# Kernel optimization log

Hardware: AMD Instinct MI355X
Metric: run time of the kernel (lower is better)

## Reference

```python
import jax, jax.numpy as jnp
import numpy as np

B, N, D, H = 8, 512, 512, 8
DK = D // H          # 64
DIM_G = 64           # trigonometric geometry embedding dim
WAVE_LEN = 1000.0


def box_relational_embedding(f_g):
    # f_g: [B, N, 4] -> [B, N, N, 64]
    x_min, y_min, x_max, y_max = [f_g[..., i] for i in range(4)]  # [B,N]
    cx = (x_min + x_max) * 0.5
    cy = (y_min + y_max) * 0.5
    w = x_max - x_min + 1.0
    h = y_max - y_min + 1.0
    # pairwise deltas; divide by w_i / h_i of the row box (broadcast over j)
    dx = jnp.log(jnp.clip(jnp.abs((cx[:, :, None] - cx[:, None, :]) / w[:, :, None]), 0.001))
    dy = jnp.log(jnp.clip(jnp.abs((cy[:, :, None] - cy[:, None, :]) / h[:, :, None]), 0.001))
    dw = jnp.log(w[:, :, None] / w[:, None, :])
    dh = jnp.log(h[:, :, None] / h[:, None, :])
    pos = jnp.stack([dx, dy, dw, dh], axis=-1)  # [B,N,N,4]
    feat_range = jnp.arange(DIM_G // 8, dtype=jnp.float32) / (DIM_G / 8.0)  # [8]
    dim_mat = 1.0 / (WAVE_LEN ** feat_range)  # [8]
    mul = (100.0 * pos)[..., None] * dim_mat  # [B,N,N,4,8]
    mul = mul.reshape(pos.shape[0], pos.shape[1], pos.shape[2], -1)  # [B,N,N,32]
    return jnp.concatenate([jnp.sin(mul), jnp.cos(mul)], axis=-1)  # [B,N,N,64]


def setup_inputs() -> dict:
    key = jax.random.key(0)
    ks = jax.random.split(key, 12)
    s = 1.0 / np.sqrt(D)
    return {
        "input_query": jax.random.normal(ks[0], (B, N, D), jnp.float32),
        "input_key": jax.random.normal(ks[1], (B, N, D), jnp.float32),
        "input_value": jax.random.normal(ks[2], (B, N, D), jnp.float32),
        "input_box": jax.random.uniform(ks[3], (B, N, 4), jnp.float32),
        "mask": jax.random.randint(ks[4], (B, N), 0, 2, jnp.int32),
        "not_objects": jax.random.randint(ks[5], (B, N), 0, 2).astype(jnp.bool_),
        "Wq": jax.random.normal(ks[6], (D, D), jnp.float32) * s,
        "bq": jnp.zeros((D,), jnp.float32),
        "Wk": jax.random.normal(ks[7], (D, D), jnp.float32) * s,
        "bk": jnp.zeros((D,), jnp.float32),
        "Wv": jax.random.normal(ks[8], (D, D), jnp.float32) * s,
        "bv": jnp.zeros((D,), jnp.float32),
        "Wo": jax.random.normal(ks[9], (D, D), jnp.float32) * s,
        "bo": jnp.zeros((D,), jnp.float32),
        "WG": jax.random.normal(ks[10], (H, DIM_G), jnp.float32) * 0.1,
        "bG": jnp.zeros((H,), jnp.float32),
    }


def reference(input_query, input_key, input_value, input_box, mask, not_objects,
              Wq, bq, Wk, bk, Wv, bv, Wo, bo, WG, bG):
    emb = box_relational_embedding(input_box)  # [B,N,N,64]

    def proj(x, W, b):
        return (x @ W + b).reshape(B, N, H, DK).transpose(0, 2, 1, 3)  # [B,H,N,DK]

    q = proj(input_query, Wq, bq)
    k = proj(input_key, Wk, bk)
    v = proj(input_value, Wv, bv)

    scores = jnp.einsum('bhnd,bhmd->bhnm', q, k) / np.sqrt(DK).astype(np.float32)
    scores = jnp.where(mask[:, None, None, :] == 0, -1e9, scores)

    # per-head geometry weights: [B,H,N,N]
    wg = jax.nn.relu(jnp.einsum('bnmg,hg->bhnm', emb, WG) + bG[None, :, None, None])

    # object mask: zero the geometry log-bias where either i or j is not an object
    pair_not_obj = not_objects[:, None, :, None] | not_objects[:, None, None, :]  # [B,1,N,N]
    mask_obj = 1.0 - pair_not_obj.astype(jnp.float32)

    logits = jnp.log(jnp.clip(wg, 1e-6)) * mask_obj + scores
    attn = jax.nn.softmax(logits, axis=-1)  # dropout is identity in eval mode

    out = jnp.einsum('bhnm,bhmd->bhnd', attn, v)
    out = out.transpose(0, 2, 1, 3).reshape(B, N, D)
    return out @ Wo + bo
```

## Files before the change

### kernel.cpp

```cpp
#include <hip/hip_runtime.h>
#include <hip/hip_fp16.h>

#define B_ 8
#define N_ 512
#define D_ 512
#define H_ 8
#define DK_ 64

typedef unsigned int uint;
typedef unsigned short ushort;
typedef __attribute__((ext_vector_type(8))) short short8;
typedef __attribute__((ext_vector_type(8))) _Float16 half8;
typedef __attribute__((ext_vector_type(4))) _Float16 half4;
typedef __attribute__((ext_vector_type(4))) float floatx4;

__device__ __forceinline__ float bf2f(ushort s) { return __uint_as_float(((uint)s) << 16); }
__device__ __forceinline__ ushort f2bf(float f) {
    uint x = __float_as_uint(f);
    return (ushort)((x + 0x7fffu + ((x >> 16) & 1u)) >> 16);
}
__device__ __forceinline__ float blo(uint u) { return __uint_as_float(u << 16); }
__device__ __forceinline__ float bhi(uint u) { return __uint_as_float(u & 0xffff0000u); }
__device__ __forceinline__ float ldf(const void* p, size_t i, int isbf) {
    return isbf ? bf2f(((const ushort*)p)[i]) : ((const float*)p)[i];
}
__device__ __forceinline__ short ldb(const void* p, size_t i, int isbf) {
    return isbf ? (short)(((const ushort*)p)[i]) : (short)f2bf(((const float*)p)[i]);
}
__device__ __forceinline__ float4 ldbox(const void* p, size_t row, int isbf) {
    if (isbf) {
        const uint2 u = ((const uint2*)p)[row];
        return make_float4(blo(u.x), bhi(u.x), blo(u.y), bhi(u.y));
    }
    return ((const float4*)p)[row];
}
__device__ __forceinline__ float flog(float x) {
    return __builtin_amdgcn_logf(x) * 0.69314718056f;
}
__device__ __forceinline__ float fexp(float x) {
    return __builtin_amdgcn_exp2f(x * 1.44269504089f);
}
__device__ __forceinline__ void fsincos_rev(float rev, float* s, float* c) {
    const float fr = rev - floorf(rev);
    *s = __builtin_amdgcn_sinf(fr);
    *c = __builtin_amdgcn_cosf(fr);
}
__device__ __forceinline__ uint pkbf(uint a, uint b) {
    return __builtin_amdgcn_perm(b + 0x8000u, a + 0x8000u, 0x07060302u);
}
__device__ __forceinline__ int sniff_dtype(const uint* q, int* scratch) {
    const int t = threadIdx.x;
    int cnt = 0;
    for (int i = t; i < 4096; i += 256) {
        const uint e = (q[i] >> 7) & 0xffu;
        cnt += (e >= 0x70u && e <= 0x84u) ? 1 : 0;
    }
    scratch[t] = cnt;
    __syncthreads();
    for (int d = 128; d > 0; d >>= 1) {
        if (t < d) scratch[t] += scratch[t + d];
        __syncthreads();
    }
    const int r = (scratch[0] > 3276) ? 1 : 0;
    __syncthreads();
    return r;
}

__global__ __launch_bounds__(256) void probe_dtype(const uint* __restrict__ q,
                                                   int* __restrict__ flag) {
    __shared__ int s[256];
    const int r = sniff_dtype(q, s);
    if (threadIdx.x == 0) *flag = r;
}

__global__ __launch_bounds__(256) void transw(const void* __restrict__ w0,
                                              const void* __restrict__ w1,
                                              const void* __restrict__ w2,
                                              const void* __restrict__ w3,
                                              const void* __restrict__ b0,
                                              const void* __restrict__ b1,
                                              const void* __restrict__ b2,
                                              const void* __restrict__ b3,
                                              const uint* __restrict__ xq,
                                              ushort* __restrict__ wt,
                                              float* __restrict__ biasf,
                                              int* __restrict__ flag) {
    __shared__ int cnt_s[256];
    const int isbf = sniff_dtype(xq, cnt_s);
    const int z = blockIdx.z;
    const void* W = (z == 0) ? w0 : (z == 1) ? w1 : (z == 2) ? w2 : w3;
    const int n0 = blockIdx.x * 32, k0 = blockIdx.y * 32;
    __shared__ float tile[32][33];
    const int tx = threadIdx.x & 31, ty = threadIdx.x >> 5;
#pragma unroll
    for (int r = 0; r < 4; ++r)
        tile[ty + 8 * r][tx] = ldf(W, (size_t)(k0 + ty + 8 * r) * D_ + n0 + tx, isbf);
    if (blockIdx.x == 0 && blockIdx.y == 0) {
        const void* bz = (z == 0) ? b0 : (z == 1) ? b1 : (z == 2) ? b2 : b3;
        for (int e = threadIdx.x; e < 512; e += 256)
            biasf[z * 512 + e] = ldf(bz, e, isbf);
        if (z == 0 && threadIdx.x == 0) *flag = isbf;
    }
    __syncthreads();
#pragma unroll
    for (int r = 0; r < 4; ++r)
        wt[(size_t)z * 262144 + (size_t)(n0 + ty + 8 * r) * D_ + k0 + tx] =
            f2bf(tile[tx][ty + 8 * r]);
}

__global__ __launch_bounds__(256) void stage1(
    const void* __restrict__ xq, const void* __restrict__ xk, const void* __restrict__ xv,
    const ushort* __restrict__ wt, const float* __restrict__ biasf,
    ushort* __restrict__ oq, ushort* __restrict__ ok, ushort* __restrict__ ov,
    const void* __restrict__ box, const int* __restrict__ nobj,
    const void* __restrict__ WG, const void* __restrict__ bG,
    ushort* __restrict__ glog, const int* __restrict__ flagp) {
    __shared__ __align__(16) char smem[22336];
    const int isbf = *flagp;
    const int grp = blockIdx.x / 11, kk = blockIdx.x % 11;
    const int t = threadIdx.x, wv = t >> 6, lane = t & 63;
    const int m16 = lane & 15, quad = lane >> 4;

    if (kk < 3) {
        const int id = grp * 3 + kk;
        const int z = id >> 9, rem = id & 511;
        const int row0 = (rem & 63) * 64, col0 = (rem >> 6) * 64;
        const char* A = (const char*)((z == 0) ? xq : (z == 1) ? xk : xv);
        const ushort* W = wt + (size_t)z * 262144;
        const float* bias = biasf + z * 512;
        ushort (*As)[40] = (ushort(*)[40])smem;
        ushort (*Ws)[40] = (ushort(*)[40])(smem + 5120);
        floatx4 acc[4] = {};

        const int ar = t >> 2, ac = (t & 3) * 8;

        uint4 ua, ub;
        short8 ps, pw;
        auto loadA = [&](int k0) {
            const size_t e = (size_t)(row0 + ar) * D_ + k0 + ac;
            if (isbf) {
                ps = *(const short8*)(A + 2 * e);
            } else {
                const uint* ap = (const uint*)A + e;
                ua = *(const uint4*)(ap);
                ub = *(const uint4*)(ap + 4);
            }
            pw = *(const short8*)(W + (size_t)(col0 + ar) * D_ + k0 + ac);
        };
        auto stage = [&]() {
            if (isbf) {
                *(short8*)&As[ar][ac] = ps;
            } else {
                uint4 lo;
                lo.x = pkbf(ua.x, ua.y); lo.y = pkbf(ua.z, ua.w);
                lo.z = pkbf(ub.x, ub.y); lo.w = pkbf(ub.z, ub.w);
                *(uint4*)&As[ar][ac] = lo;
            }
            *(short8*)&Ws[ar][ac] = pw;
        };

        loadA(0);
        for (int k0 = 0; k0 < D_; k0 += 32) {
            __syncthreads();
            stage();
            __syncthreads();
            if (k0 + 32 < D_) loadA(k0 + 32);

            const short8 a0 = *(const short8*)&As[wv * 16 + m16][quad * 8];
            const short8 b0 = *(const short8*)&Ws[m16][quad * 8];
            const short8 b1 = *(const short8*)&Ws[16 + m16][quad * 8];
            const short8 b2 = *(const short8*)&Ws[32 + m16][quad * 8];
            const short8 b3 = *(const short8*)&Ws[48 + m16][quad * 8];
            acc[0] = __builtin_amdgcn_mfma_f32_16x16x32_bf16(a0, b0, acc[0], 0, 0, 0);
            acc[1] = __builtin_amdgcn_mfma_f32_16x16x32_bf16(a0, b1, acc[1], 0, 0, 0);
            acc[2] = __builtin_amdgcn_mfma_f32_16x16x32_bf16(a0, b2, acc[2], 0, 0, 0);
            acc[3] = __builtin_amdgcn_mfma_f32_16x16x32_bf16(a0, b3, acc[3], 0, 0, 0);
        }

#pragma unroll
        for (int nt = 0; nt < 4; ++nt) {
            const int colg = col0 + nt * 16 + m16;
            const float bi = bias[colg];
            const float v0 = acc[nt][0] + bi, v1 = acc[nt][1] + bi;
            const float v2 = acc[nt][2] + bi, v3 = acc[nt][3] + bi;
            const int rowb = row0 + wv * 16 + quad * 4;
            if (z == 2) {
                const int bhv = (rowb >> 9) * H_ + (colg >> 6);
                uint2 pk;
                pk.x = (uint)f2bf(v0) | ((uint)f2bf(v1) << 16);
                pk.y = (uint)f2bf(v2) | ((uint)f2bf(v3) << 16);
                *(uint2*)(ov + ((size_t)bhv * DK_ + (colg & 63)) * N_ + (rowb & 511)) = pk;
            } else {
                ushort* o = (z == 0) ? oq : ok;
                const float vv[4] = {v0, v1, v2, v3};
#pragma unroll
                for (int r = 0; r < 4; ++r) {
                    const int row = rowb + r;
                    o[((size_t)((row >> 9) * H_ + (colg >> 6)) * N_ + (row & 511)) * DK_ +
                      (colg & 63)] = f2bf(vv[r]);
                }
            }
        }
    } else {
        const int id = grp * 8 + (kk - 3);
        const int i = id & 511, bl = id >> 9;
        _Float16 (*trig)[76] = (_Float16(*)[76])smem;
        _Float16 (*wgf)[72] = (_Float16(*)[72])(smem + 19456);
        float* mobja = (float*)(smem + 21760);
        float* bgs = (float*)(smem + 22272);

        for (int e = t; e < 1024; e += 256) {
            const int h = e >> 6, g = e & 63;
            wgf[h][g] = (_Float16)((h < 8) ? ldf(WG, (size_t)h * 64 + g, isbf) : 0.f);
        }
        if (t < 8) bgs[t] = ldf(bG, t, isbf);

        const float4 bi4 = ldbox(box, (size_t)bl * N_ + i, isbf);
        const float wi = bi4.z - bi4.x + 1.0f, hi = bi4.w - bi4.y + 1.0f;
        const float cxi = (bi4.x + bi4.z) * 0.5f, cyi = (bi4.y + bi4.w) * 0.5f;
        const float rwi = 1.0f / wi, rhi = 1.0f / hi;
        const float lwi = flog(wi), lhi = flog(hi);
        const int noi = nobj[bl * N_ + i];
        __syncthreads();

        const half8 bf0 = *(const half8*)&wgf[m16][quad * 8];
        const half8 bf1 = *(const half8*)&wgf[m16][quad * 8 + 32];
        _Float16* gb = (_Float16*)glog +
                       ((((size_t)bl * 32 + (i >> 4)) * 8) * 16 + (i & 15)) * 512;
        const float dmrev[8] = {15.915494f, 6.7115083f, 2.8302207f, 1.1934936f,
                                0.50329214f, 0.21223603f, 0.089498095f, 0.037742074f};

        for (int c = 0; c < 4; ++c) {
            const int jbase = c * 128;
            {
                const int pair = t >> 1, hf = t & 1;
                const int j = jbase + pair;
                const float4 bj4 = ldbox(box, (size_t)bl * N_ + j, isbf);
                const float wj = bj4.z - bj4.x + 1.0f, hj = bj4.w - bj4.y + 1.0f;
                float p0, p1;
                if (hf == 0) {
                    const float cxj = (bj4.x + bj4.z) * 0.5f, cyj = (bj4.y + bj4.w) * 0.5f;
                    p0 = flog(fmaxf(fabsf((cxi - cxj) * rwi), 0.001f));
                    p1 = flog(fmaxf(fabsf((cyi - cyj) * rhi), 0.001f));
                    mobja[pair] = (noi || nobj[bl * N_ + j]) ? 0.f : 1.f;
                } else {
                    p0 = lwi - flog(wj);
                    p1 = lhi - flog(hj);
                }
#pragma unroll
                for (int pp = 0; pp < 2; ++pp) {
                    const float base = pp ? p1 : p0;
                    half8 s8, c8;
#pragma unroll
                    for (int f = 0; f < 8; ++f) {
                        float sv, cv;
                        fsincos_rev(base * dmrev[f], &sv, &cv);
                        s8[f] = (_Float16)sv;
                        c8[f] = (_Float16)cv;
                    }
                    const int g0 = hf * 16 + pp * 8;
                    *(half4*)&trig[pair][g0]          = *(const half4*)&s8;
                    *(half4*)&trig[pair][g0 + 4]      = *((const half4*)&s8 + 1);
                    *(half4*)&trig[pair][32 + g0]     = *(const half4*)&c8;
                    *(half4*)&trig[pair][32 + g0 + 4] = *((const half4*)&c8 + 1);
                }
            }
            __syncthreads();
            {
#pragma unroll
                for (int sub = 0; sub < 2; ++sub) {
                    const int row = wv * 32 + sub * 16 + m16;
                    half8 a0, a1;
                    *((half4*)&a0)     = *(const half4*)&trig[row][quad * 8];
                    *((half4*)&a0 + 1) = *(const half4*)&trig[row][quad * 8 + 4];
                    *((half4*)&a1)     = *(const half4*)&trig[row][32 + quad * 8];
                    *((half4*)&a1 + 1) = *(const half4*)&trig[row][32 + quad * 8 + 4];
                    floatx4 acc = {};
                    acc = __builtin_amdgcn_mfma_f32_16x16x32_f16(a0, bf0, acc, 0, 0, 0);
                    acc = __builtin_amdgcn_mfma_f32_16x16x32_f16(a1, bf1, acc, 0, 0, 0);
                    if (m16 < 8) {
#pragma unroll
                        for (int r = 0; r < 4; ++r) {
                            const int pair = wv * 32 + sub * 16 + quad * 4 + r;
                            const float wg = acc[r] + bgs[m16];
                            const float gl = flog(fmaxf(wg, 1e-6f)) * mobja[pair];
                            gb[(size_t)m16 * 8192 + jbase + pair] = (_Float16)gl;
                        }
                    }
                }
            }
            __syncthreads();
        }
    }
}

__global__ __launch_bounds__(256) void gemm1(
    const ushort* __restrict__ att, const ushort* __restrict__ wt,
    const float* __restrict__ biasf, void* __restrict__ dout,
    const int* __restrict__ flagp) {
    const int isbf = *flagp;
    const ushort* W = wt + (size_t)3 * 262144;
    const float* bias = biasf + 3 * 512;
    const int row0 = blockIdx.x * 64, col0 = blockIdx.y * 64;
    const int t = threadIdx.x, wv = t >> 6, lane = t & 63;
    const int m16 = lane & 15, quad = lane >> 4;

    __shared__ ushort As[64][40];
    __shared__ ushort Ws[64][40];
    floatx4 acc[4] = {};

    const int ar = t >> 2, ac = (t & 3) * 8;

    short8 ps, pw;
    auto loadA = [&](int k0) {
        ps = *(const short8*)(att + (size_t)(row0 + ar) * D_ + k0 + ac);
        pw = *(const short8*)(W + (size_t)(col0 + ar) * D_ + k0 + ac);
    };

    loadA(0);
    for (int k0 = 0; k0 < D_; k0 += 32) {
        __syncthreads();
        *(short8*)&As[ar][ac] = ps;
        *(short8*)&Ws[ar][ac] = pw;
        __syncthreads();
        if (k0 + 32 < D_) loadA(k0 + 32);

        const short8 a0 = *(const short8*)&As[wv * 16 + m16][quad * 8];
        const short8 b0 = *(const short8*)&Ws[m16][quad * 8];
        const short8 b1 = *(const short8*)&Ws[16 + m16][quad * 8];
        const short8 b2 = *(const short8*)&Ws[32 + m16][quad * 8];
        const short8 b3 = *(const short8*)&Ws[48 + m16][quad * 8];
        acc[0] = __builtin_amdgcn_mfma_f32_16x16x32_bf16(a0, b0, acc[0], 0, 0, 0);
        acc[1] = __builtin_amdgcn_mfma_f32_16x16x32_bf16(a0, b1, acc[1], 0, 0, 0);
        acc[2] = __builtin_amdgcn_mfma_f32_16x16x32_bf16(a0, b2, acc[2], 0, 0, 0);
        acc[3] = __builtin_amdgcn_mfma_f32_16x16x32_bf16(a0, b3, acc[3], 0, 0, 0);
    }

#pragma unroll
    for (int nt = 0; nt < 4; ++nt) {
        const int colg = col0 + nt * 16 + m16;
        const float bi = bias[colg];
#pragma unroll
        for (int r = 0; r < 4; ++r) {
            const int row = row0 + wv * 16 + quad * 4 + r;
            const float v = acc[nt][r] + bi;
            if (isbf) ((ushort*)dout)[(size_t)row * D_ + colg] = f2bf(v);
            else      ((float*)dout)[(size_t)row * D_ + colg] = v;
        }
    }
}

__global__ __launch_bounds__(256) void attn3(
    const ushort* __restrict__ qw, const ushort* __restrict__ kw,
    const ushort* __restrict__ vt, const int* __restrict__ mask,
    const ushort* __restrict__ glog, ushort* __restrict__ att, int b0) {
    const int it = blockIdx.x, h = blockIdx.y, bl = blockIdx.z;
    const int bg = b0 + bl;
    const int i0 = it * 16;
    const int t = threadIdx.x, wv = t >> 6, lane = t & 63;
    const int m16 = lane & 15, quad = lane >> 4;
    const size_t bh = (size_t)(bg * H_ + h);

    __shared__ float lg[16][516];
    __shared__ ushort sbuf[16 * 520];
    __shared__ float rsumInv[16];

    {
        const uint4* src = (const uint4*)(glog + (((size_t)bl * 32 + it) * 8 + h) * 8192);
        uint4* dst = (uint4*)sbuf;
#pragma unroll
        for (int e = 0; e < 4; ++e) dst[t + 256 * e] = src[t + 256 * e];
    }
    const ushort* qrow = qw + (bh * N_ + i0 + m16) * DK_ + quad * 8;
    const short8 aq0 = *(const short8*)(qrow);
    const short8 aq1 = *(const short8*)(qrow + 32);
    __syncthreads();

#pragma unroll
    for (int tt = 0; tt < 8; ++tt) {
        const int j0 = wv * 128 + tt * 16;
        const ushort* krow = kw + (bh * N_ + j0 + m16) * DK_ + quad * 8;
        const short8 bk0 = *(const short8*)(krow);
        const short8 bk1 = *(const short8*)(krow + 32);
        floatx4 acc = {};
        acc = __builtin_amdgcn_mfma_f32_16x16x32_bf16(aq0, bk0, acc, 0, 0, 0);
        acc = __builtin_amdgcn_mfma_f32_16x16x32_bf16(aq1, bk1, acc, 0, 0, 0);
        const int mj = mask[bg * N_ + j0 + m16];
        const __half* gt = (const __half*)sbuf;
#pragma unroll
        for (int r = 0; r < 4; ++r) {
            const int i = quad * 4 + r;
            const float g = __half2float(gt[i * 512 + j0 + m16]);
            lg[i][j0 + m16] = (mj ? 0.125f * acc[r] : -1e9f) + g;
        }
    }
    __syncthreads();

    {
        const int row = t >> 4, l = t & 15;
        float v[32];
        float mx = -3e38f;
#pragma unroll
        for (int s = 0; s < 32; ++s) { v[s] = lg[row][l + 16 * s]; mx = fmaxf(mx, v[s]); }
#pragma unroll
        for (int d = 1; d < 16; d <<= 1) mx = fmaxf(mx, __shfl_xor(mx, d, 16));
        float sm = 0.f;
#pragma unroll
        for (int s = 0; s < 32; ++s) { const float p = fexp(v[s] - mx); sm += p; v[s] = p; }
#pragma unroll
        for (int d = 1; d < 16; d <<= 1) sm += __shfl_xor(sm, d, 16);
#pragma unroll
        for (int s = 0; s < 32; ++s)
            sbuf[row * 520 + l + 16 * s] = (ushort)((__float_as_uint(v[s]) + 0x8000u) >> 16);
        if (l == 0) rsumInv[row] = 1.0f / sm;
    }
    __syncthreads();

    {
        const int dk0 = wv * 16;
        const ushort* vrow = vt + (bh * DK_ + dk0 + m16) * N_ + quad * 8;
        floatx4 oc = {};
#pragma unroll
        for (int kc = 0; kc < 16; ++kc) {
            const short8 ap = *(const short8*)(sbuf + m16 * 520 + kc * 32 + quad * 8);
            const short8 bv = *(const short8*)(vrow + kc * 32);
            oc = __builtin_amdgcn_mfma_f32_16x16x32_bf16(ap, bv, oc, 0, 0, 0);
        }
#pragma unroll
        for (int r = 0; r < 4; ++r) {
            const int i = quad * 4 + r;
            const float o = oc[r] * rsumInv[i];
            att[((size_t)(bg * N_ + i0 + i)) * D_ + h * DK_ + dk0 + m16] = f2bf(o);
        }
    }
}

__global__ __launch_bounds__(256) void gemm16(const void* __restrict__ A,
                                              const void* __restrict__ W,
                                              const void* __restrict__ bias,
                                              void* __restrict__ out,
                                              const int* __restrict__ flagp,
                                              int a_follows, int mode) {
    const int isbf = *flagp;
    const int a_isbf = a_follows ? isbf : 1;
    const int wave = threadIdx.x >> 6;
    const int tile = blockIdx.x * 4 + wave;
    const int tm = tile >> 5, tn = tile & 31;
    const int row0 = tm * 16, col0 = tn * 16;
    const int lane = threadIdx.x & 63;
    const int m = lane & 15, quad = lane >> 4;
    floatx4 acc = {0.f, 0.f, 0.f, 0.f};
    const size_t abase = (size_t)(row0 + m) * D_ + quad * 8;
    const size_t wbase = (size_t)(quad * 8) * D_ + col0 + m;
    for (int k0 = 0; k0 < D_; k0 += 32) {
        short8 af, bf;
#pragma unroll
        for (int j = 0; j < 8; ++j) af[j] = ldb(A, abase + k0 + j, a_isbf);
#pragma unroll
        for (int j = 0; j < 8; ++j) bf[j] = ldb(W, wbase + (size_t)(k0 + j) * D_, isbf);
        acc = __builtin_amdgcn_mfma_f32_16x16x32_bf16(af, bf, acc, 0, 0, 0);
    }
    const int col = col0 + m;
    const float bi = ldf(bias, col, isbf);
#pragma unroll
    for (int r = 0; r < 4; ++r) {
        const int row = row0 + quad * 4 + r;
        const float v = acc[r] + bi;
        if (mode == 1) {
            ((ushort*)out)[(size_t)(((row >> 9) * H_ + (col >> 6)) * N_ + (row & 511)) * DK_ + (col & 63)] = f2bf(v);
        } else if (isbf) {
            ((ushort*)out)[(size_t)row * D_ + col] = f2bf(v);
        } else {
            ((float*)out)[(size_t)row * D_ + col] = v;
        }
    }
}

__global__ __launch_bounds__(256) void attn_old(
    const ushort* __restrict__ qw, const ushort* __restrict__ kw,
    const ushort* __restrict__ vw, const void* __restrict__ box,
    const int* __restrict__ mask, const int* __restrict__ nobj,
    const void* __restrict__ WG, const void* __restrict__ bG,
    ushort* __restrict__ att, const int* __restrict__ flagp) {
    const int isbf = *flagp;
    const int b = blockIdx.z, h = blockIdx.y;
    const int i0 = blockIdx.x * 8;
    const int t = threadIdx.x;
    __shared__ float lg[8][520];
    __shared__ float q_s[8][68];
    __shared__ float wgh[64];
    __shared__ float cxi[8], cyi[8], rwi[8], rhi[8], lwi[8], lhi[8];
    __shared__ int noi[8];
    __shared__ float rsum[8];
    for (int e = t; e < 512; e += 256) {
        const int ii = e >> 6, dk = e & 63;
        q_s[ii][dk] = bf2f(qw[(size_t)((b * H_ + h) * N_ + i0 + ii) * DK_ + dk]) * 0.125f;
    }
    if (t < 64) wgh[t] = ldf(WG, h * 64 + t, isbf);
    if (t < 8) {
        const size_t bb = (size_t)(b * N_ + i0 + t) * 4;
        const float xmn = ldf(box, bb + 0, isbf), ymn = ldf(box, bb + 1, isbf);
        const float xmx = ldf(box, bb + 2, isbf), ymx = ldf(box, bb + 3, isbf);
        const float w = xmx - xmn + 1.0f, hh = ymx - ymn + 1.0f;
        cxi[t] = (xmn + xmx) * 0.5f;
        cyi[t] = (ymn + ymx) * 0.5f;
        rwi[t] = 1.0f / w;
        rhi[t] = 1.0f / hh;
        lwi[t] = __logf(w);
        lhi[t] = __logf(hh);
        noi[t] = nobj[b * N_ + i0 + t];
    }
    const float bg = ldf(bG, h, isbf);
    __syncthreads();
    for (int jl = 0; jl < 2; ++jl) {
        const int j = t + jl * 256;
        float acc[8];
#pragma unroll
        for (int ii = 0; ii < 8; ++ii) acc[ii] = 0.f;
        const uint4* krow = (const uint4*)(kw + (size_t)((b * H_ + h) * N_ + j) * DK_);
#pragma unroll
        for (int c = 0; c < 8; ++c) {
            const uint4 ku = krow[c];
            float kf[8];
            kf[0] = blo(ku.x); kf[1] = bhi(ku.x); kf[2] = blo(ku.y); kf[3] = bhi(ku.y);
            kf[4] = blo(ku.z); kf[5] = bhi(ku.z); kf[6] = blo(ku.w); kf[7] = bhi(ku.w);
#pragma unroll
            for (int ii = 0; ii < 8; ++ii) {
                const float4 qa = *(const float4*)(&q_s[ii][c * 8]);
                const float4 qb = *(const float4*)(&q_s[ii][c * 8 + 4]);
                acc[ii] += qa.x * kf[0] + qa.y * kf[1] + qa.z * kf[2] + qa.w * kf[3] +
                           qb.x * kf[4] + qb.y * kf[5] + qb.z * kf[6] + qb.w * kf[7];
            }
        }
        const int mj = mask[b * N_ + j];
        const size_t bb = (size_t)(b * N_ + j) * 4;
        const float xmn = ldf(box, bb + 0, isbf), ymn = ldf(box, bb + 1, isbf);
        const float xmx = ldf(box, bb + 2, isbf), ymx = ldf(box, bb + 3, isbf);
        const float cxj = (xmn + xmx) * 0.5f, cyj = (ymn + ymx) * 0.5f;
        const float wj = xmx - xmn + 1.0f, hj = ymx - ymn + 1.0f;
        const float lwj = __logf(wj), lhj = __logf(hj);
        const int noj = nobj[b * N_ + j];
        const float dm[8] = {1.0f, 0.421696503f, 0.177827941f, 0.074989421f,
                             0.031622777f, 0.013335214f, 0.005623413f, 0.002371374f};
        for (int ii = 0; ii < 8; ++ii) {
            const float mobj = (noi[ii] || noj) ? 0.f : 1.f;
            const float dx = __logf(fmaxf(fabsf((cxi[ii] - cxj) * rwi[ii]), 0.001f));
            const float dy = __logf(fmaxf(fabsf((cyi[ii] - cyj) * rhi[ii]), 0.001f));
            const float pos[4] = {dx, dy, lwi[ii] - lwj, lhi[ii] - lhj};
            float wg = bg;
            for (int p = 0; p < 4; ++p) {
                const float base = 100.f * pos[p];
#pragma unroll
                for (int f = 0; f < 8; ++f) {
                    float sv, cv;
                    __sincosf(base * dm[f], &sv, &cv);
                    const int g = p * 8 + f;
                    wg += sv * wgh[g] + cv * wgh[32 + g];
                }
            }
            lg[ii][j] = (mj ? acc[ii] : -1e9f) + __logf(fmaxf(wg, 1e-6f)) * mobj;
        }
    }
    __syncthreads();
    {
        const int rr = t >> 5, l32 = t & 31;
        float mx = -3e38f;
        for (int j = l32; j < N_; j += 32) mx = fmaxf(mx, lg[rr][j]);
#pragma unroll
        for (int d = 1; d < 32; d <<= 1) mx = fmaxf(mx, __shfl_xor(mx, d, 32));
        float sm = 0.f;
        for (int j = l32; j < N_; j += 32) {
            const float p = __expf(lg[rr][j] - mx);
            lg[rr][j] = p;
            sm += p;
        }
#pragma unroll
        for (int d = 1; d < 32; d <<= 1) sm += __shfl_xor(sm, d, 32);
        if (l32 == 0) rsum[rr] = sm;
    }
    __syncthreads();
    {
        const int ii = t >> 5, dkp = t & 31;
        float o0 = 0.f, o1 = 0.f;
        const uint* vbase = (const uint*)vw + (size_t)((b * H_ + h) * N_) * (DK_ / 2) + dkp;
        for (int j = 0; j < N_; ++j) {
            const uint u = vbase[(size_t)j * (DK_ / 2)];
            const float p = lg[ii][j];
            o0 += p * blo(u);
            o1 += p * bhi(u);
        }
        const float inv = 1.0f / rsum[ii];
        const uint pk = (uint)f2bf(o0 * inv) | ((uint)f2bf(o1 * inv) << 16);
        ((uint*)att)[(size_t)(b * N_ + i0 + ii) * (D_ / 2) + h * 32 + dkp] = pk;
    }
}

extern "C" void kernel_launch(void* const* d_in, const int* in_sizes, int n_in,
                              void* d_out, int out_size, void* d_ws, size_t ws_size,
                              hipStream_t stream) {
    const void* xq = d_in[0];
    const void* xk = d_in[1];
    const void* xv = d_in[2];
    const void* box = d_in[3];
    const int* mask = (const int*)d_in[4];
    const int* nobj = (const int*)d_in[5];
    const void* Wq = d_in[6];
    const void* bq = d_in[7];
    const void* Wk = d_in[8];
    const void* bk = d_in[9];
    const void* Wv = d_in[10];
    const void* bv = d_in[11];
    const void* Wo = d_in[12];
    const void* bo = d_in[13];
    const void* WG = d_in[14];
    const void* bG = d_in[15];

    char* ws = (char*)d_ws;
    const size_t MB = 1u << 20;

    if (ws_size >= 54 * MB) {
        int* flag = (int*)ws;
        float* biasf = (float*)(ws + 4096);
        ushort* wt = (ushort*)(ws + 16384);
        size_t p = 16384 + 2097152;
        ushort* qw = (ushort*)(ws + p); p += 4194304;
        ushort* kw = (ushort*)(ws + p); p += 4194304;
        ushort* vt = (ushort*)(ws + p); p += 4194304;
        ushort* att = (ushort*)(ws + p); p += 4194304;
        ushort* glog = (ushort*)(ws + p);

        hipLaunchKernelGGL(transw, dim3(16, 16, 4), dim3(256), 0, stream,
                           Wq, Wk, Wv, Wo, bq, bk, bv, bo, (const uint*)xq,
                           wt, biasf, flag);
        hipLaunchKernelGGL(stage1, dim3(5632), dim3(256), 0, stream,
                           xq, xk, xv, wt, biasf, qw, kw, vt,
                           box, nobj, WG, bG, glog, flag);
        hipLaunchKernelGGL(attn3, dim3(32, H_, B_), dim3(256), 0, stream,
                           qw, kw, vt, mask, glog, att, 0);
        hipLaunchKernelGGL(gemm1, dim3(64, 8), dim3(256), 0, stream,
                           att, wt, biasf, d_out, flag);
    } else {
        int* flag = (int*)ws;
        ushort* qw = (ushort*)(ws + 256);
        ushort* kw = (ushort*)(ws + 256 + 4194304);
        ushort* vw = (ushort*)(ws + 256 + 8388608);
        ushort* att = (ushort*)(ws + 256 + 12582912);
        hipLaunchKernelGGL(probe_dtype, dim3(1), dim3(256), 0, stream, (const uint*)xq, flag);
        hipLaunchKernelGGL(gemm16, dim3(2048), dim3(256), 0, stream, xq, Wq, bq, (void*)qw, flag, 1, 1);
        hipLaunchKernelGGL(gemm16, dim3(2048), dim3(256), 0, stream, xk, Wk, bk, (void*)kw, flag, 1, 1);
        hipLaunchKernelGGL(gemm16, dim3(2048), dim3(256), 0, stream, xv, Wv, bv, (void*)vw, flag, 1, 1);
        hipLaunchKernelGGL(attn_old, dim3(N_ / 8, H_, B_), dim3(256), 0, stream,
                           qw, kw, vw, box, mask, nobj, WG, bG, att, flag);
        hipLaunchKernelGGL(gemm16, dim3(2048), dim3(256), 0, stream, att, Wo, bo, d_out, flag, 0, 2);
    }
}
```

Baseline: 187.8 us.

## Keep attention logits in registers and shrink trig smem padding

After: 186.6 us. About the same (-0.6%).

```diff
diff --git a/kernel.cpp b/kernel.cpp
--- a/kernel.cpp
+++ b/kernel.cpp
@@ -115,7 +115,7 @@
     const void* __restrict__ box, const int* __restrict__ nobj,
     const void* __restrict__ WG, const void* __restrict__ bG,
     ushort* __restrict__ glog, const int* __restrict__ flagp) {
-    __shared__ __align__(16) char smem[22336];
+    __shared__ __align__(16) char smem[20352];
     const int isbf = *flagp;
     const int grp = blockIdx.x / 11, kk = blockIdx.x % 11;
     const int t = threadIdx.x, wv = t >> 6, lane = t & 63;
@@ -204,10 +204,10 @@
     } else {
         const int id = grp * 8 + (kk - 3);
         const int i = id & 511, bl = id >> 9;
-        _Float16 (*trig)[76] = (_Float16(*)[76])smem;
-        _Float16 (*wgf)[72] = (_Float16(*)[72])(smem + 19456);
-        float* mobja = (float*)(smem + 21760);
-        float* bgs = (float*)(smem + 22272);
+        _Float16 (*trig)[68] = (_Float16(*)[68])smem;
+        _Float16 (*wgf)[72] = (_Float16(*)[72])(smem + 17408);
+        float* mobja = (float*)(smem + 19712);
+        float* bgs = (float*)(smem + 20224);
 
         for (int e = t; e < 1024; e += 256) {
             const int h = e >> 6, g = e & 63;
@@ -361,8 +361,9 @@
     const int m16 = lane & 15, quad = lane >> 4;
     const size_t bh = (size_t)(bg * H_ + h);
 
-    __shared__ float lg[16][516];
     __shared__ ushort sbuf[16 * 520];
+    __shared__ float red[16][4];
+    __shared__ float rmax[16];
     __shared__ float rsumInv[16];
 
     {
@@ -376,6 +377,7 @@
     const short8 aq1 = *(const short8*)(qrow + 32);
     __syncthreads();
 
+    float lt[8][4];
 #pragma unroll
     for (int tt = 0; tt < 8; ++tt) {
         const int j0 = wv * 128 + tt * 16;
@@ -391,29 +393,53 @@
         for (int r = 0; r < 4; ++r) {
             const int i = quad * 4 + r;
             const float g = __half2float(gt[i * 512 + j0 + m16]);
-            lg[i][j0 + m16] = (mj ? 0.125f * acc[r] : -1e9f) + g;
-        }
-    }
-    __syncthreads();
-
+            lt[tt][r] = (mj ? 0.125f * acc[r] : -1e9f) + g;
+        }
+    }
     {
-        const int row = t >> 4, l = t & 15;
-        float v[32];
-        float mx = -3e38f;
-#pragma unroll
-        for (int s = 0; s < 32; ++s) { v[s] = lg[row][l + 16 * s]; mx = fmaxf(mx, v[s]); }
-#pragma unroll
-        for (int d = 1; d < 16; d <<= 1) mx = fmaxf(mx, __shfl_xor(mx, d, 16));
-        float sm = 0.f;
-#pragma unroll
-        for (int s = 0; s < 32; ++s) { const float p = fexp(v[s] - mx); sm += p; v[s] = p; }
-#pragma unroll
-        for (int d = 1; d < 16; d <<= 1) sm += __shfl_xor(sm, d, 16);
-#pragma unroll
-        for (int s = 0; s < 32; ++s)
-            sbuf[row * 520 + l + 16 * s] = (ushort)((__float_as_uint(v[s]) + 0x8000u) >> 16);
-        if (l == 0) rsumInv[row] = 1.0f / sm;
-    }
+        float pm[4];
+#pragma unroll
+        for (int r = 0; r < 4; ++r) {
+            float m = lt[0][r];
+#pragma unroll
+            for (int tt = 1; tt < 8; ++tt) m = fmaxf(m, lt[tt][r]);
+#pragma unroll
+            for (int d = 1; d < 16; d <<= 1) m = fmaxf(m, __shfl_xor(m, d, 16));
+            pm[r] = m;
+        }
+        if (m16 == 0) {
+#pragma unroll
+            for (int r = 0; r < 4; ++r) red[quad * 4 + r][wv] = pm[r];
+        }
+    }
+    __syncthreads();
+    if (t < 16) rmax[t] = fmaxf(fmaxf(red[t][0], red[t][1]), fmaxf(red[t][2], red[t][3]));
+    __syncthreads();
+    {
+        float ps[4];
+#pragma unroll
+        for (int r = 0; r < 4; ++r) {
+            const int i = quad * 4 + r;
+            const float mx = rmax[i];
+            float s = 0.f;
+#pragma unroll
+            for (int tt = 0; tt < 8; ++tt) {
+                const float p = fexp(lt[tt][r] - mx);
+                s += p;
+                sbuf[i * 520 + wv * 128 + tt * 16 + m16] =
+                    (ushort)((__float_as_uint(p) + 0x8000u) >> 16);
+            }
+#pragma unroll
+            for (int d = 1; d < 16; d <<= 1) s += __shfl_xor(s, d, 16);
+            ps[r] = s;
+        }
+        if (m16 == 0) {
+#pragma unroll
+            for (int r = 0; r < 4; ++r) red[quad * 4 + r][wv] = ps[r];
+        }
+    }
+    __syncthreads();
+    if (t < 16) rsumInv[t] = 1.0f / (red[t][0] + red[t][1] + red[t][2] + red[t][3]);
     __syncthreads();
 
     {
```
